# Kernel tuning notes

Hardware: AMD Instinct MI355X
Metric: run time of the kernel (lower is better)

Reference implementation:

```python
import jax, jax.numpy as jnp
import numpy as np


def setup_inputs() -> dict:
    key = jax.random.key(0)
    k1, k2 = jax.random.split(key)
    B, C = 32, 256
    H = W = 512
    NUM_LABELS = 150  # label values in [0, 150), so unique count <= 150 < C
    cls_score = jax.random.normal(k1, (B, C), dtype=jnp.float32)
    label = jax.random.randint(k2, (B, H, W), 0, NUM_LABELS, dtype=jnp.int64)
    return {"cls_score": cls_score, "label": label}


def reference(cls_score, label):
    # Count unique label values per sample.
    # torch.unique(label.reshape(B,-1), dim=-1) followed by per-row torch.unique
    # is equivalent to: sort each row, count value changes + 1.
    B = label.shape[0]
    lab = label.reshape(B, -1)                      # [B, N]
    s = jnp.sort(lab, axis=-1)                      # segmented sort per row
    counts = 1 + jnp.sum(s[:, 1:] != s[:, :-1], axis=-1)  # [B] int, #unique per row
    # F.cross_entropy(cls_score, counts): mean of -log_softmax at target index
    logp = jax.nn.log_softmax(cls_score, axis=-1)   # [B, C]
    nll = -jnp.take_along_axis(logp, counts[:, None], axis=-1)[:, 0]  # [B]
    return jnp.mean(nll)
```

## Files before the change

kernel.cpp:

```cpp
#include <hip/hip_runtime.h>
#include <hip/hip_bf16.h>


#define B_SAMPLES 32
#define C_CLASSES 256
#define N_PER_SAMPLE (512 * 512)
#define CHUNKS 16
#define PER_CHUNK (N_PER_SAMPLE / CHUNKS)

__global__ __launch_bounds__(256) void count_bitmap_kernel(
    const int* __restrict__ label, unsigned long long* __restrict__ masks) {
    const int b = blockIdx.x / CHUNKS;
    const int chunk = blockIdx.x % CHUNKS;
    const int t = threadIdx.x;

    __shared__ int flag[C_CLASSES];
    flag[t] = 0;
    __syncthreads();

    const int4* p = reinterpret_cast<const int4*>(
        label + (long)b * N_PER_SAMPLE + (long)chunk * PER_CHUNK);

    int4 v[16];
    #pragma unroll
    for (int i = 0; i < 16; ++i) v[i] = p[i * 256 + t];

    #pragma unroll
    for (int i = 0; i < 16; ++i) {
        flag[v[i].x & 255] = 1;
        flag[v[i].y & 255] = 1;
        flag[v[i].z & 255] = 1;
        flag[v[i].w & 255] = 1;
    }
    __syncthreads();

    unsigned long long m = __ballot(flag[t] != 0);
    if ((t & 63) == 0) {
        masks[(unsigned)blockIdx.x * 4 + (t >> 6)] = m;
    }
}

__global__ __launch_bounds__(256) void ce_kernel(
    const float* __restrict__ cls,
    const unsigned long long* __restrict__ masks,
    float* __restrict__ out) {
    const int t = threadIdx.x;
    const int w = t >> 6;
    const int l = t & 63;

    __shared__ int cnt_sh[B_SAMPLES];
    __shared__ float partial[4];

    float4 v[8];
    #pragma unroll
    for (int i = 0; i < 8; ++i) {
        const int b = w * 8 + i;
        v[i] = reinterpret_cast<const float4*>(cls)[b * 64 + l];
    }

    if (t < 128) {
        const int b    = t >> 2;
        const int word = t & 3;
        const unsigned long long* base = masks + ((unsigned)(b * CHUNKS)) * 4 + word;

        unsigned long long acc = 0ull;
        #pragma unroll
        for (int jj = 0; jj < 2; ++jj) {
            const unsigned long long x0 = base[(jj * 8 + 0) * 4];
            const unsigned long long x1 = base[(jj * 8 + 1) * 4];
            const unsigned long long x2 = base[(jj * 8 + 2) * 4];
            const unsigned long long x3 = base[(jj * 8 + 3) * 4];
            const unsigned long long x4 = base[(jj * 8 + 4) * 4];
            const unsigned long long x5 = base[(jj * 8 + 5) * 4];
            const unsigned long long x6 = base[(jj * 8 + 6) * 4];
            const unsigned long long x7 = base[(jj * 8 + 7) * 4];
            acc |= ((x0 | x1) | (x2 | x3)) | ((x4 | x5) | (x6 | x7));
        }

        int p = __popcll(acc);
        p += __shfl_xor(p, 1);
        p += __shfl_xor(p, 2);
        if ((t & 3) == 0) cnt_sh[t >> 2] = p;
    }
    __syncthreads();

    float nll = 0.0f;
    #pragma unroll
    for (int i = 0; i < 8; ++i) {
        const int b = w * 8 + i;
        const float4 x = v[i];
        float m = fmaxf(fmaxf(x.x, x.y), fmaxf(x.z, x.w));
        #pragma unroll
        for (int off = 32; off > 0; off >>= 1) m = fmaxf(m, __shfl_xor(m, off));
        float e = expf(x.x - m) + expf(x.y - m) + expf(x.z - m) + expf(x.w - m);
        #pragma unroll
        for (int off = 32; off > 0; off >>= 1) e += __shfl_xor(e, off);
        const float lse = m + logf(e);

        const int cnt = cnt_sh[b];
        const int comp = cnt & 3;
        const float cand = (comp == 0) ? x.x : (comp == 1) ? x.y
                         : (comp == 2) ? x.z : x.w;
        const float target = __shfl(cand, cnt >> 2);
        nll += lse - target;
    }

    if (l == 0) partial[w] = nll;
    __syncthreads();
    if (t == 0) out[0] = (partial[0] + partial[1] + partial[2] + partial[3]) / (float)B_SAMPLES;
}

extern "C" void kernel_launch(void* const* d_in, const int* in_sizes, int n_in,
                              void* d_out, int out_size, void* d_ws, size_t ws_size,
                              hipStream_t stream) {
    const float* cls = (const float*)d_in[0];
    const int* label = (const int*)d_in[1];
    float* out = (float*)d_out;
    unsigned long long* masks = (unsigned long long*)d_ws;

    count_bitmap_kernel<<<B_SAMPLES * CHUNKS, 256, 0, stream>>>(label, masks);
    ce_kernel<<<1, 256, 0, stream>>>(cls, masks, out);
}
```

Baseline: 16.66 us.

## Fuse bitmap and cross-entropy kernels via cooperative grid sync

Merges the two launches into one cooperative kernel. All 512 blocks build their per-chunk label bitmaps, then a grid-wide barrier runs and block 0 alone computes the counts and the cross-entropy. This is meant to remove the second launch and the gap between kernels. The cost is a cooperative launch and a grid.sync, which has its own overhead and needs every block to be resident at once.

```diff
diff --git a/kernel.cpp b/kernel.cpp
--- a/kernel.cpp
+++ b/kernel.cpp
@@ -1,5 +1,8 @@
 #include <hip/hip_runtime.h>
 #include <hip/hip_bf16.h>
+#include <hip/hip_cooperative_groups.h>
+
+namespace cg = cooperative_groups;
 
 
 #define B_SAMPLES 32
@@ -7,12 +10,14 @@
 #define N_PER_SAMPLE (512 * 512)
 #define CHUNKS 16
 #define PER_CHUNK (N_PER_SAMPLE / CHUNKS)
+#define NBLK (B_SAMPLES * CHUNKS)
 
-__global__ __launch_bounds__(256) void count_bitmap_kernel(
-    const int* __restrict__ label, unsigned long long* __restrict__ masks) {
+__global__ __launch_bounds__(256) void fused_coop_kernel(
+    const int* __restrict__ label, const float* __restrict__ cls,
+    unsigned long long* __restrict__ masks, float* __restrict__ out) {
+    const int t = threadIdx.x;
     const int b = blockIdx.x / CHUNKS;
     const int chunk = blockIdx.x % CHUNKS;
-    const int t = threadIdx.x;
 
     __shared__ int flag[C_CLASSES];
     flag[t] = 0;
@@ -38,66 +43,63 @@
     if ((t & 63) == 0) {
         masks[(unsigned)blockIdx.x * 4 + (t >> 6)] = m;
     }
-}
 
-__global__ __launch_bounds__(256) void ce_kernel(
-    const float* __restrict__ cls,
-    const unsigned long long* __restrict__ masks,
-    float* __restrict__ out) {
-    const int t = threadIdx.x;
-    const int w = t >> 6;
-    const int l = t & 63;
+    cg::this_grid().sync();
+
+    if (blockIdx.x != 0) return;
 
     __shared__ int cnt_sh[B_SAMPLES];
     __shared__ float partial[4];
 
-    float4 v[8];
+    const int w = t >> 6;
+    const int l = t & 63;
+
+    float4 x8[8];
     #pragma unroll
     for (int i = 0; i < 8; ++i) {
-        const int b = w * 8 + i;
-        v[i] = reinterpret_cast<const float4*>(cls)[b * 64 + l];
+        x8[i] = reinterpret_cast<const float4*>(cls)[(w * 8 + i) * 64 + l];
     }
 
     if (t < 128) {
-        const int b    = t >> 2;
+        const int bb   = t >> 2;
         const int word = t & 3;
-        const unsigned long long* base = masks + ((unsigned)(b * CHUNKS)) * 4 + word;
+        const unsigned long long* base = masks + ((unsigned)(bb * CHUNKS)) * 4 + word;
 
         unsigned long long acc = 0ull;
         #pragma unroll
         for (int jj = 0; jj < 2; ++jj) {
-            const unsigned long long x0 = base[(jj * 8 + 0) * 4];
-            const unsigned long long x1 = base[(jj * 8 + 1) * 4];
-            const unsigned long long x2 = base[(jj * 8 + 2) * 4];
-            const unsigned long long x3 = base[(jj * 8 + 3) * 4];
-            const unsigned long long x4 = base[(jj * 8 + 4) * 4];
-            const unsigned long long x5 = base[(jj * 8 + 5) * 4];
-            const unsigned long long x6 = base[(jj * 8 + 6) * 4];
-            const unsigned long long x7 = base[(jj * 8 + 7) * 4];
-            acc |= ((x0 | x1) | (x2 | x3)) | ((x4 | x5) | (x6 | x7));
+            const unsigned long long y0 = base[(jj * 8 + 0) * 4];
+            const unsigned long long y1 = base[(jj * 8 + 1) * 4];
+            const unsigned long long y2 = base[(jj * 8 + 2) * 4];
+            const unsigned long long y3 = base[(jj * 8 + 3) * 4];
+            const unsigned long long y4 = base[(jj * 8 + 4) * 4];
+            const unsigned long long y5 = base[(jj * 8 + 5) * 4];
+            const unsigned long long y6 = base[(jj * 8 + 6) * 4];
+            const unsigned long long y7 = base[(jj * 8 + 7) * 4];
+            acc |= ((y0 | y1) | (y2 | y3)) | ((y4 | y5) | (y6 | y7));
         }
 
-        int p = __popcll(acc);
-        p += __shfl_xor(p, 1);
-        p += __shfl_xor(p, 2);
-        if ((t & 3) == 0) cnt_sh[t >> 2] = p;
+        int pc = __popcll(acc);
+        pc += __shfl_xor(pc, 1);
+        pc += __shfl_xor(pc, 2);
+        if ((t & 3) == 0) cnt_sh[t >> 2] = pc;
     }
     __syncthreads();
 
     float nll = 0.0f;
     #pragma unroll
     for (int i = 0; i < 8; ++i) {
-        const int b = w * 8 + i;
-        const float4 x = v[i];
-        float m = fmaxf(fmaxf(x.x, x.y), fmaxf(x.z, x.w));
+        const int bb = w * 8 + i;
+        const float4 x = x8[i];
+        float mx = fmaxf(fmaxf(x.x, x.y), fmaxf(x.z, x.w));
         #pragma unroll
-        for (int off = 32; off > 0; off >>= 1) m = fmaxf(m, __shfl_xor(m, off));
-        float e = expf(x.x - m) + expf(x.y - m) + expf(x.z - m) + expf(x.w - m);
+        for (int off = 32; off > 0; off >>= 1) mx = fmaxf(mx, __shfl_xor(mx, off));
+        float e = expf(x.x - mx) + expf(x.y - mx) + expf(x.z - mx) + expf(x.w - mx);
         #pragma unroll
         for (int off = 32; off > 0; off >>= 1) e += __shfl_xor(e, off);
-        const float lse = m + logf(e);
+        const float lse = mx + logf(e);
 
-        const int cnt = cnt_sh[b];
+        const int cnt = cnt_sh[bb];
         const int comp = cnt & 3;
         const float cand = (comp == 0) ? x.x : (comp == 1) ? x.y
                          : (comp == 2) ? x.z : x.w;
@@ -113,11 +115,12 @@
 extern "C" void kernel_launch(void* const* d_in, const int* in_sizes, int n_in,
                               void* d_out, int out_size, void* d_ws, size_t ws_size,
                               hipStream_t stream) {
+    const int* label = (const int*)d_in[1];
     const float* cls = (const float*)d_in[0];
-    const int* label = (const int*)d_in[1];
     float* out = (float*)d_out;
     unsigned long long* masks = (unsigned long long*)d_ws;
 
-    count_bitmap_kernel<<<B_SAMPLES * CHUNKS, 256, 0, stream>>>(label, masks);
-    ce_kernel<<<1, 256, 0, stream>>>(cls, masks, out);
+    void* args[] = { (void*)&label, (void*)&cls, (void*)&masks, (void*)&out };
+    hipLaunchCooperativeKernel((void*)fused_coop_kernel,
+                               dim3(NBLK), dim3(256), args, 0, stream);
 }
```

After: 61.47 us. 269% more time.
